# Performance work log

Hardware: AMD Instinct MI355X
Metric: run time of the kernel (lower is better)

## Reference

```python
import jax, jax.numpy as jnp
import numpy as np

DIM = 1024
HEADS = 16
HIDDEN = 4 * DIM


def layernorm(x, g, b, eps=1e-5):
    mu = jnp.mean(x, axis=-1, keepdims=True)
    var = jnp.mean(jnp.square(x - mu), axis=-1, keepdims=True)
    return (x - mu) * jax.lax.rsqrt(var + eps) * g + b


def setup_inputs() -> dict:
    key = jax.random.key(0)
    ks = jax.random.split(key, 8)
    s = DIM ** -0.5
    return {
        "x": jax.random.normal(ks[0], (2, 2048, DIM), dtype=jnp.float32),
        "ln1_g": jnp.ones((DIM,), jnp.float32),
        "ln1_b": jnp.zeros((DIM,), jnp.float32),
        "qkv_w": jax.random.normal(ks[1], (DIM, 3 * DIM), jnp.float32) * s,
        "proj_w": jax.random.normal(ks[2], (DIM, DIM), jnp.float32) * s,
        "proj_b": jnp.zeros((DIM,), jnp.float32),
        "ln2_g": jnp.ones((DIM,), jnp.float32),
        "ln2_b": jnp.zeros((DIM,), jnp.float32),
        "fc1_w": jax.random.normal(ks[3], (DIM, HIDDEN), jnp.float32) * s,
        "fc1_b": jnp.zeros((HIDDEN,), jnp.float32),
        "fc2_w": jax.random.normal(ks[4], (HIDDEN, DIM), jnp.float32) * (HIDDEN ** -0.5),
        "fc2_b": jnp.zeros((DIM,), jnp.float32),
    }


def block_fwd(x, ln1_g, ln1_b, qkv_w, proj_w, proj_b, ln2_g, ln2_b,
              fc1_w, fc1_b, fc2_w, fc2_b):
    B, N, C = x.shape
    H = HEADS
    Dh = C // H
    scale = Dh ** -0.5
    # --- attention branch (pre-norm) ---
    h = layernorm(x, ln1_g, ln1_b)
    qkv = h @ qkv_w                     # [B,N,3C] (no bias: qkv_bias=False)
    qkv = qkv.reshape(B, N, 3, H, Dh)
    q = qkv[:, :, 0].transpose(0, 2, 1, 3)   # [B,H,N,Dh]
    k = qkv[:, :, 1].transpose(0, 2, 1, 3)
    v = qkv[:, :, 2].transpose(0, 2, 1, 3)
    attn = jnp.einsum('bhqd,bhkd->bhqk', q, k) * scale
    attn = jax.nn.softmax(attn, axis=-1)
    o = jnp.einsum('bhqk,bhkd->bhqd', attn, v)
    o = o.transpose(0, 2, 1, 3).reshape(B, N, C)
    x = x + (o @ proj_w + proj_b)
    # --- MLP branch (pre-norm) ---
    h = layernorm(x, ln2_g, ln2_b)
    h = jax.nn.gelu(h @ fc1_w + fc1_b, approximate=False)  # torch nn.GELU = exact erf
    x = x + (h @ fc2_w + fc2_b)
    return x


def reference(x, ln1_g, ln1_b, qkv_w, proj_w, proj_b, ln2_g, ln2_b,
              fc1_w, fc1_b, fc2_w, fc2_b):
    return block_fwd(x, ln1_g, ln1_b, qkv_w, proj_w, proj_b, ln2_g, ln2_b,
                     fc1_w, fc1_b, fc2_w, fc2_b)
```

## Files before the change

kernel.cpp:

```cpp
#include <hip/hip_runtime.h>
#include <math.h>

typedef unsigned short u16;
typedef unsigned int u32;
typedef __attribute__((ext_vector_type(8))) short short8;
typedef __attribute__((ext_vector_type(4))) float f32x4;
typedef __attribute__((ext_vector_type(16))) float f32x16;
typedef __attribute__((ext_vector_type(2))) u32 u32x2;
typedef __attribute__((ext_vector_type(4))) u32 u32x4;
typedef __attribute__((ext_vector_type(4))) u16 u16x4;

typedef __attribute__((address_space(1))) const void gmem_t;
typedef __attribute__((address_space(3))) void lmem_t;

__device__ __forceinline__ u16 f2bf(float f) {
  u32 u = __builtin_bit_cast(u32, f);
  u = u + 0x7fffu + ((u >> 16) & 1u);
  return (u16)(u >> 16);
}

__device__ __forceinline__ u32 cvt_pk_bf16(float a, float b) {
  u32 r;
  asm("v_cvt_pk_bf16_f32 %0, %1, %2" : "=v"(r) : "v"(a), "v"(b));
  return r;
}

__device__ __forceinline__ void g2l16(const void* g, void* l) {
  __builtin_amdgcn_global_load_lds((gmem_t*)g, (lmem_t*)l, 16, 0, 0);
}

template <int N> __device__ __forceinline__ void waitcnt_vm() {
  if constexpr (N == 0)      asm volatile("s_waitcnt vmcnt(0)" ::: "memory");
  else if constexpr (N == 4) asm volatile("s_waitcnt vmcnt(4)" ::: "memory");
  else if constexpr (N == 6) asm volatile("s_waitcnt vmcnt(6)" ::: "memory");
  else if constexpr (N == 8) asm volatile("s_waitcnt vmcnt(8)" ::: "memory");
  else static_assert(N == 0 || N == 4 || N == 6 || N == 8, "add literal");
}

__global__ __launch_bounds__(256) void wtrans_all(
    const float* __restrict__ qkvw, const float* __restrict__ projw,
    const float* __restrict__ fc1w, const float* __restrict__ fc2w,
    u16* __restrict__ o_qkv, u16* __restrict__ o_proj,
    u16* __restrict__ o_fc1, u16* __restrict__ o_fc2) {
  int id = (int)blockIdx.x;
  const float* in; u16* out; int R, C, bid;
  if (id < 768)       { in = qkvw;  out = o_qkv;  R = 1024; C = 3072; bid = id; }
  else if (id < 1024) { in = projw; out = o_proj; R = 1024; C = 1024; bid = id - 768; }
  else if (id < 2048) { in = fc1w;  out = o_fc1;  R = 1024; C = 4096; bid = id - 1024; }
  else                { in = fc2w;  out = o_fc2;  R = 4096; C = 1024; bid = id - 2048; }
  __shared__ float t[64][65];
  int tid = threadIdx.x;
  int nbx = C >> 6;
  int bx = bid % nbx, by = bid / nbx;
  int r0 = by << 6, c0 = bx << 6;
  int lr = tid >> 2, lc = (tid & 3) << 4;
  const float* src = in + (size_t)(r0 + lr) * C + c0 + lc;
#pragma unroll
  for (int j = 0; j < 4; ++j) {
    f32x4 v = *(const f32x4*)(src + j * 4);
    t[lr][lc + j * 4 + 0] = v.x; t[lr][lc + j * 4 + 1] = v.y;
    t[lr][lc + j * 4 + 2] = v.z; t[lr][lc + j * 4 + 3] = v.w;
  }
  __syncthreads();
  int oc = tid >> 2, orr = (tid & 3) << 4;
  u16* dst = out + (size_t)(c0 + oc) * R + r0 + orr;
  u32 u[8];
#pragma unroll
  for (int j = 0; j < 8; ++j)
    u[j] = (u32)f2bf(t[orr + 2 * j][oc]) | ((u32)f2bf(t[orr + 2 * j + 1][oc]) << 16);
  u32x4 v0; v0.x = u[0]; v0.y = u[1]; v0.z = u[2]; v0.w = u[3];
  u32x4 v1; v1.x = u[4]; v1.y = u[5]; v1.z = u[6]; v1.w = u[7];
  *(u32x4*)(dst) = v0;
  *(u32x4*)(dst + 8) = v1;
}

__global__ __launch_bounds__(256) void lnorm(const float* __restrict__ in,
                                             const float* __restrict__ gw,
                                             const float* __restrict__ bw,
                                             u16* __restrict__ out) {
  int r = blockIdx.x, tid = threadIdx.x;
  const f32x4 v = *((const f32x4*)(in + (size_t)r * 1024) + tid);
  float s = v.x + v.y + v.z + v.w;
  float ss = v.x * v.x + v.y * v.y + v.z * v.z + v.w * v.w;
#pragma unroll
  for (int o = 32; o >= 1; o >>= 1) { s += __shfl_xor(s, o); ss += __shfl_xor(ss, o); }
  __shared__ float red[8];
  int w = tid >> 6;
  if ((tid & 63) == 0) { red[w] = s; red[4 + w] = ss; }
  __syncthreads();
  s = red[0] + red[1] + red[2] + red[3];
  ss = red[4] + red[5] + red[6] + red[7];
  float mu = s * (1.0f / 1024.0f);
  float var = ss * (1.0f / 1024.0f) - mu * mu;
  float rstd = rsqrtf(var + 1e-5f);
  const f32x4 g4 = *((const f32x4*)gw + tid);
  const f32x4 b4 = *((const f32x4*)bw + tid);
  u16x4 o;
  o.x = f2bf((v.x - mu) * rstd * g4.x + b4.x);
  o.y = f2bf((v.y - mu) * rstd * g4.y + b4.y);
  o.z = f2bf((v.z - mu) * rstd * g4.z + b4.z);
  o.w = f2bf((v.w - mu) * rstd * g4.w + b4.w);
  *((u16x4*)(out + (size_t)r * 1024) + tid) = o;
}

template <int EPI, int BM, int BN>
__global__ __launch_bounds__(256, 2) void gemm_bt(
    const u16* __restrict__ A, const u16* __restrict__ BT, int M, int N, int K,
    const float* __restrict__ bias, const float* __restrict__ resid,
    float* __restrict__ fout, u16* __restrict__ bout) {
  constexpr int AIT = BM / 32, BIT = BN / 32;
  constexpr int L = AIT + BIT;
  constexpr int MR = BM / 32, NR = BN / 32;
  __shared__ __align__(16) u16 smA[2][BM * 64];
  __shared__ __align__(16) u16 smB[2][BN * 64];
  int tid = threadIdx.x;
  int w = tid >> 6, l = tid & 63, lq = l & 15, g = l >> 4;
  int nbx = N / BN;
  int t = (int)blockIdx.x;
  int cpx = (int)gridDim.x >> 3;
  t = (t & 7) * cpx + (t >> 3);
  int by = t / nbx, bx = t - by * nbx;
  long brow = (long)by * BM, bcol = (long)bx * BN;
  int wr = w >> 1, wc = w & 1;

  const u16* aS[AIT]; const u16* bS[BIT];
#pragma unroll
  for (int it = 0; it < AIT; ++it) {
    int p = it * 256 + tid;
    int row = p >> 3;
    int gc = (p & 7) ^ (row & 7);
    aS[it] = A + (size_t)(brow + row) * K + gc * 8;
  }
#pragma unroll
  for (int it = 0; it < BIT; ++it) {
    int p = it * 256 + tid;
    int row = p >> 3;
    int gc = (p & 7) ^ (row & 7);
    bS[it] = BT + (size_t)(bcol + row) * K + gc * 8;
  }
  auto STAGE = [&](int buf, int k0) {
#pragma unroll
    for (int it = 0; it < AIT; ++it) g2l16(aS[it] + k0, &smA[buf][it * 2048 + w * 512]);
#pragma unroll
    for (int it = 0; it < BIT; ++it) g2l16(bS[it] + k0, &smB[buf][it * 2048 + w * 512]);
  };

  f32x4 zero = {0.f, 0.f, 0.f, 0.f};
  f32x4 acc[MR][NR];
#pragma unroll
  for (int m = 0; m < MR; ++m)
#pragma unroll
    for (int n = 0; n < NR; ++n) acc[m][n] = zero;

  int NT = K >> 6;
  STAGE(0, 0);
  for (int tt = 0; tt < NT; ++tt) {
    int cur = tt & 1;
    int knext = ((tt + 1) == NT ? 0 : (tt + 1)) << 6;
    STAGE(cur ^ 1, knext);
    waitcnt_vm<L>();
    __builtin_amdgcn_s_barrier();
    asm volatile("" ::: "memory");

    const char* sA = (const char*)&smA[cur][0];
    const char* sB = (const char*)&smB[cur][0];
#pragma unroll
    for (int c = 0; c < 2; ++c) {
      short8 af[MR], bfb[NR];
#pragma unroll
      for (int m = 0; m < MR; ++m) {
        int r = wr * (BM / 2) + m * 16 + lq;
        af[m] = *(const short8*)(sA + r * 128 + ((g * 16 + c * 64) ^ ((r & 7) << 4)));
      }
#pragma unroll
      for (int n = 0; n < NR; ++n) {
        int r = wc * (BN / 2) + n * 16 + lq;
        bfb[n] = *(const short8*)(sB + r * 128 + ((g * 16 + c * 64) ^ ((r & 7) << 4)));
      }
#pragma unroll
      for (int m = 0; m < MR; ++m)
#pragma unroll
        for (int n = 0; n < NR; ++n)
          acc[m][n] = __builtin_amdgcn_mfma_f32_16x16x32_bf16(af[m], bfb[n], acc[m][n], 0, 0, 0);
    }
    asm volatile("" ::: "memory");
    __builtin_amdgcn_s_barrier();
  }
  waitcnt_vm<0>();

  long colbase = bcol + wc * (BN / 2);
#pragma unroll
  for (int m = 0; m < MR; ++m) {
#pragma unroll
    for (int n = 0; n < NR; ++n) {
      f32x4 v = acc[m][n];
      long col = colbase + n * 16 + lq;
      long row0 = brow + wr * (BM / 2) + m * 16 + g * 4;
      float bb = bias[col];
#pragma unroll
      for (int i = 0; i < 4; ++i) {
        long idx = (row0 + i) * N + col;
        fout[idx] = resid[idx] + v[i] + bb;
      }
    }
  }
}

template <int EPI>
__global__ __launch_bounds__(256, 4) void gemm32(
    const u16* __restrict__ A, const u16* __restrict__ BT, int M, int N, int K,
    const float* __restrict__ bias,
    u16* __restrict__ bout, u16* __restrict__ bout2, u16* __restrict__ bout3) {
  __shared__ __align__(16) u16 smA[2][128 * 32];
  __shared__ __align__(16) u16 smB[2][128 * 32];
  int tid = threadIdx.x;
  int w = tid >> 6, l = tid & 63, lq = l & 15, g = l >> 4;
  int nbx = N >> 7;
  int t = (int)blockIdx.x;
  int cpx = (int)gridDim.x >> 3;
  t = (t & 7) * cpx + (t >> 3);
  int by = t / nbx, bx = t - by * nbx;
  long brow = (long)by << 7, bcol = (long)bx << 7;
  int wr = w >> 1, wc = w & 1;

  const u16* aS[2]; const u16* bS[2];
#pragma unroll
  for (int it = 0; it < 2; ++it) {
    int p = it * 256 + tid;
    int sp = (p & 7) ^ ((p >> 3) & 7);
    int row = ((p >> 3) << 1) | (sp >> 2);
    int c = sp & 3;
    aS[it] = A + (size_t)(brow + row) * K + c * 8;
    bS[it] = BT + (size_t)(bcol + row) * K + c * 8;
  }
  auto STAGE = [&](int buf, int k0) {
#pragma unroll
    for (int it = 0; it < 2; ++it) {
      g2l16(aS[it] + k0, &smA[buf][it * 2048 + w * 512]);
      g2l16(bS[it] + k0, &smB[buf][it * 2048 + w * 512]);
    }
  };

  f32x4 zero = {0.f, 0.f, 0.f, 0.f};
  f32x4 acc[4][4];
#pragma unroll
  for (int m = 0; m < 4; ++m)
#pragma unroll
    for (int n = 0; n < 4; ++n) acc[m][n] = zero;

  int NT = K >> 5;
  STAGE(0, 0);
  for (int tt = 0; tt < NT; ++tt) {
    int cur = tt & 1;
    int knext = ((tt + 1) == NT ? 0 : (tt + 1)) << 5;
    STAGE(cur ^ 1, knext);
    waitcnt_vm<4>();
    __builtin_amdgcn_s_barrier();
    asm volatile("" ::: "memory");

    const char* sA = (const char*)&smA[cur][0];
    const char* sB = (const char*)&smB[cur][0];
    short8 af[4], bfb[4];
#pragma unroll
    for (int m = 0; m < 4; ++m) {
      int r = wr * 64 + m * 16 + lq;
      af[m] = *(const short8*)(sA + ((r >> 1) * 128 +
                ((((r & 1) << 6) + (g << 4)) ^ (((r >> 1) & 7) << 4))));
    }
#pragma unroll
    for (int n = 0; n < 4; ++n) {
      int r = wc * 64 + n * 16 + lq;
      bfb[n] = *(const short8*)(sB + ((r >> 1) * 128 +
                ((((r & 1) << 6) + (g << 4)) ^ (((r >> 1) & 7) << 4))));
    }
    __builtin_amdgcn_s_setprio(1);
#pragma unroll
    for (int m = 0; m < 4; ++m)
#pragma unroll
      for (int n = 0; n < 4; ++n)
        acc[m][n] = __builtin_amdgcn_mfma_f32_16x16x32_bf16(af[m], bfb[n], acc[m][n], 0, 0, 0);
    __builtin_amdgcn_s_setprio(0);
    asm volatile("" ::: "memory");
    __builtin_amdgcn_s_barrier();
  }
  waitcnt_vm<0>();

#pragma unroll
  for (int m = 0; m < 4; ++m) {
#pragma unroll
    for (int n = 0; n < 4; ++n) {
      f32x4 v = acc[m][n];
      long col = bcol + wc * 64 + n * 16 + lq;
      long row0 = brow + wr * 64 + m * 16 + g * 4;
      if constexpr (EPI == 0) {
        int part = (int)(bcol >> 10);
        long colq = col - ((long)part << 10);
        int hh = (int)(colq >> 6), d = (int)(colq & 63);
#pragma unroll
        for (int i = 0; i < 4; ++i) {
          long row = row0 + i;
          long b = row >> 11, nq = row & 2047;
          long bh = b * 16 + hh;
          u16 val = f2bf(v[i]);
          if (part == 0)      bout [(bh * 2048 + nq) * 64 + d] = val;
          else if (part == 1) bout2[(bh * 2048 + nq) * 64 + d] = val;
          else                bout3[(bh * 64 + d) * 2048 + nq] = val;
        }
      } else {
        float bb = bias[col];
#pragma unroll
        for (int i = 0; i < 4; ++i) {
          float xg = v[i] + bb;
          float ge = 0.5f * xg * (1.0f + erff(xg * 0.70710678118654752f));
          bout[(row0 + i) * (long)N + col] = f2bf(ge);
        }
      }
    }
  }
}

template <int BASE>
__device__ __forceinline__ short8 mk_pfrag(const f32x16& s, float sc) {
  u32 x = cvt_pk_bf16(exp2f(s[BASE + 0] * sc - 12.0f), exp2f(s[BASE + 1] * sc - 12.0f));
  u32 y = cvt_pk_bf16(exp2f(s[BASE + 2] * sc - 12.0f), exp2f(s[BASE + 3] * sc - 12.0f));
  u32 u = cvt_pk_bf16(exp2f(s[BASE + 4] * sc - 12.0f), exp2f(s[BASE + 5] * sc - 12.0f));
  u32 v = cvt_pk_bf16(exp2f(s[BASE + 6] * sc - 12.0f), exp2f(s[BASE + 7] * sc - 12.0f));
  asm("v_permlane32_swap_b32 %0, %1" : "+v"(x), "+v"(u));
  asm("v_permlane32_swap_b32 %0, %1" : "+v"(y), "+v"(v));
  u32x4 f; f.x = x; f.y = y; f.z = u; f.w = v;
  return __builtin_bit_cast(short8, f);
}

__global__ __launch_bounds__(256, 2) void attn_fwd(const u16* __restrict__ qb,
                                                   const u16* __restrict__ kbuf,
                                                   const u16* __restrict__ vtb,
                                                   u16* __restrict__ ob) {
  __shared__ __align__(16) u16 kl[2][64 * 64];
  __shared__ __align__(16) u16 vl[2][64 * 64];
  int tid = threadIdx.x;
  int w = tid >> 6, l = tid & 63, q32 = l & 31, hi = l >> 5;
  int bh = (int)blockIdx.x & 31;
  int qt = (int)blockIdx.x >> 5;

  const u16* qp = qb + ((size_t)bh * 2048 + qt * 128 + w * 32 + q32) * 64 + hi * 8;
  short8 qf[4];
#pragma unroll
  for (int kc = 0; kc < 4; ++kc) qf[kc] = *(const short8*)(qp + kc * 16);

  const u16* kS[2]; const u16* vS[2];
#pragma unroll
  for (int it = 0; it < 2; ++it) {
    int p = it * 256 + tid;
    int row = p >> 3;
    int gc = (p & 7) ^ (row & 7);
    kS[it] = kbuf + ((size_t)bh * 2048 + row) * 64 + gc * 8;
    vS[it] = vtb + ((size_t)bh * 64 + row) * 2048 + gc * 8;
  }
  auto issue = [&](int buf, int kt0) {
#pragma unroll
    for (int it = 0; it < 2; ++it) {
      g2l16(kS[it] + (size_t)kt0 * 64, &kl[buf][it * 2048 + w * 512]);
      g2l16(vS[it] + kt0,              &vl[buf][it * 2048 + w * 512]);
    }
  };

  f32x16 z16 = {0,0,0,0,0,0,0,0,0,0,0,0,0,0,0,0};
  f32x16 accO0 = z16, accO1 = z16, accl = z16;
  const float sc = 0.125f * 1.44269504088896f;
  u32x4 ov; ov.x = ov.y = ov.z = ov.w = 0x3F803F80u;
  short8 onesf = __builtin_bit_cast(short8, ov);
  int swz = (q32 & 7) << 4;

  issue(0, 0);
  for (int t = 0; t < 32; ++t) {
    int cur = t & 1;
    issue(cur ^ 1, ((t + 1) & 31) << 6);
    waitcnt_vm<4>();
    __builtin_amdgcn_s_barrier();
    asm volatile("" ::: "memory");

    const char* klc = (const char*)&kl[cur][0];
    const char* vlc = (const char*)&vl[cur][0];

    f32x16 s0 = z16, s1 = z16;
    __builtin_amdgcn_s_setprio(1);
#pragma unroll
    for (int kc = 0; kc < 4; ++kc) {
      short8 k0 = *(const short8*)(klc + (q32 * 128 +        ((kc * 32 + hi * 16) ^ swz)));
      short8 k1 = *(const short8*)(klc + ((32 + q32) * 128 + ((kc * 32 + hi * 16) ^ swz)));
      s0 = __builtin_amdgcn_mfma_f32_32x32x16_bf16(k0, qf[kc], s0, 0, 0, 0);
      s1 = __builtin_amdgcn_mfma_f32_32x32x16_bf16(k1, qf[kc], s1, 0, 0, 0);
    }
    __builtin_amdgcn_s_setprio(0);

    short8 pf0 = mk_pfrag<0>(s0, sc);
    short8 pf1 = mk_pfrag<8>(s0, sc);
    short8 pf2 = mk_pfrag<0>(s1, sc);
    short8 pf3 = mk_pfrag<8>(s1, sc);

    short8 va0[4], va1[4];
#pragma unroll
    for (int c = 0; c < 4; ++c) {
      va0[c] = *(const short8*)(vlc + (q32 * 128 +        ((c * 32 + hi * 16) ^ swz)));
      va1[c] = *(const short8*)(vlc + ((32 + q32) * 128 + ((c * 32 + hi * 16) ^ swz)));
    }
    __builtin_amdgcn_s_setprio(1);
    accO0 = __builtin_amdgcn_mfma_f32_32x32x16_bf16(va0[0], pf0, accO0, 0, 0, 0);
    accO1 = __builtin_amdgcn_mfma_f32_32x32x16_bf16(va1[0], pf0, accO1, 0, 0, 0);
    accl  = __builtin_amdgcn_mfma_f32_32x32x16_bf16(onesf,  pf0, accl,  0, 0, 0);
    accO0 = __builtin_amdgcn_mfma_f32_32x32x16_bf16(va0[1], pf1, accO0, 0, 0, 0);
    accO1 = __builtin_amdgcn_mfma_f32_32x32x16_bf16(va1[1], pf1, accO1, 0, 0, 0);
    accl  = __builtin_amdgcn_mfma_f32_32x32x16_bf16(onesf,  pf1, accl,  0, 0, 0);
    accO0 = __builtin_amdgcn_mfma_f32_32x32x16_bf16(va0[2], pf2, accO0, 0, 0, 0);
    accO1 = __builtin_amdgcn_mfma_f32_32x32x16_bf16(va1[2], pf2, accO1, 0, 0, 0);
    accl  = __builtin_amdgcn_mfma_f32_32x32x16_bf16(onesf,  pf2, accl,  0, 0, 0);
    accO0 = __builtin_amdgcn_mfma_f32_32x32x16_bf16(va0[3], pf3, accO0, 0, 0, 0);
    accO1 = __builtin_amdgcn_mfma_f32_32x32x16_bf16(va1[3], pf3, accO1, 0, 0, 0);
    accl  = __builtin_amdgcn_mfma_f32_32x32x16_bf16(onesf,  pf3, accl,  0, 0, 0);
    __builtin_amdgcn_s_setprio(0);

    asm volatile("" ::: "memory");
    __builtin_amdgcn_s_barrier();
  }
  waitcnt_vm<0>();

  float li = 1.0f / accl[0];
  int b = bh >> 4, h = bh & 15;
  long q = (long)qt * 128 + w * 32 + q32;
  u16* obase = ob + ((long)b * 2048 + q) * 1024 + h * 64;
#pragma unroll
  for (int j = 0; j < 8; ++j) {
    int d = ((2 * j) & 3) + 8 * (j >> 1) + 4 * hi;
    *(u32*)(obase + d)      = cvt_pk_bf16(accO0[2 * j] * li, accO0[2 * j + 1] * li);
    *(u32*)(obase + 32 + d) = cvt_pk_bf16(accO1[2 * j] * li, accO1[2 * j + 1] * li);
  }
}

extern "C" void kernel_launch(void* const* d_in, const int* in_sizes, int n_in,
                              void* d_out, int out_size, void* d_ws, size_t ws_size,
                              hipStream_t stream) {
  const float* x     = (const float*)d_in[0];
  const float* ln1g  = (const float*)d_in[1];
  const float* ln1b  = (const float*)d_in[2];
  const float* qkvw  = (const float*)d_in[3];
  const float* projw = (const float*)d_in[4];
  const float* projb = (const float*)d_in[5];
  const float* ln2g  = (const float*)d_in[6];
  const float* ln2b  = (const float*)d_in[7];
  const float* fc1w  = (const float*)d_in[8];
  const float* fc1b  = (const float*)d_in[9];
  const float* fc2w  = (const float*)d_in[10];
  const float* fc2b  = (const float*)d_in[11];
  char* ws = (char*)d_ws;
  u16* qkv_wt  = (u16*)(ws + 0);
  u16* proj_wt = (u16*)(ws + 6291456);
  u16* fc1_wt  = (u16*)(ws + 8388608);
  u16* fc2_wt  = (u16*)(ws + 16777216);
  u16* h       = (u16*)(ws + 25165824);
  u16* qbuf    = (u16*)(ws + 33554432);
  u16* kbuf    = (u16*)(ws + 41943040);
  u16* vtbuf   = (u16*)(ws + 50331648);
  u16* aout    = (u16*)(ws + 58720256);
  float* y1    = (float*)(ws + 67108864);
  u16* gbuf    = (u16*)(ws + 33554432);
  float* outp  = (float*)d_out;

  wtrans_all<<<3072, 256, 0, stream>>>(qkvw, projw, fc1w, fc2w,
                                       qkv_wt, proj_wt, fc1_wt, fc2_wt);

  lnorm<<<4096, 256, 0, stream>>>(x, ln1g, ln1b, h);
  gemm32<0><<<768, 256, 0, stream>>>(h, qkv_wt, 4096, 3072, 1024,
                                     nullptr, qbuf, kbuf, vtbuf);
  attn_fwd<<<512, 256, 0, stream>>>(qbuf, kbuf, vtbuf, aout);
  gemm_bt<1, 64, 128><<<512, 256, 0, stream>>>(aout, proj_wt, 4096, 1024, 1024,
                                               projb, x, y1, nullptr);
  lnorm<<<4096, 256, 0, stream>>>(y1, ln2g, ln2b, h);
  gemm32<2><<<1024, 256, 0, stream>>>(h, fc1_wt, 4096, 4096, 1024,
                                      fc1b, gbuf, nullptr, nullptr);
  gemm_bt<3, 64, 128><<<512, 256, 0, stream>>>(gbuf, fc2_wt, 4096, 1024, 4096,
                                               fc2b, y1, outp, nullptr);
}
```

Baseline: 246.1 us.

## Split attention over key halves and add a combine kernel

Attention blocks now each process half of the key sequence, doubling the grid so more blocks are resident per CU, and write unnormalised bf16 partial outputs plus row sums to scratch. A new combine kernel sums the two partials and normalises. The softmax scale is folded into Q during the QKV GEMM epilogue, removing a multiply-add per score. This adds an extra launch, a scratch write and read of the partial outputs, and a small extra bf16 rounding of the partials.

```diff
diff --git a/kernel.cpp b/kernel.cpp
--- a/kernel.cpp
+++ b/kernel.cpp
@@ -36,6 +36,8 @@
   else if constexpr (N == 8) asm volatile("s_waitcnt vmcnt(8)" ::: "memory");
   else static_assert(N == 0 || N == 4 || N == 6 || N == 8, "add literal");
 }
+
+#define QSCALE 0.1803368801111204f
 
 __global__ __launch_bounds__(256) void wtrans_all(
     const float* __restrict__ qkvw, const float* __restrict__ projw,
@@ -301,10 +303,9 @@
           long row = row0 + i;
           long b = row >> 11, nq = row & 2047;
           long bh = b * 16 + hh;
-          u16 val = f2bf(v[i]);
-          if (part == 0)      bout [(bh * 2048 + nq) * 64 + d] = val;
-          else if (part == 1) bout2[(bh * 2048 + nq) * 64 + d] = val;
-          else                bout3[(bh * 64 + d) * 2048 + nq] = val;
+          if (part == 0)      bout [(bh * 2048 + nq) * 64 + d] = f2bf(v[i] * QSCALE);
+          else if (part == 1) bout2[(bh * 2048 + nq) * 64 + d] = f2bf(v[i]);
+          else                bout3[(bh * 64 + d) * 2048 + nq] = f2bf(v[i]);
         }
       } else {
         float bb = bias[col];
@@ -320,27 +321,30 @@
 }
 
 template <int BASE>
-__device__ __forceinline__ short8 mk_pfrag(const f32x16& s, float sc) {
-  u32 x = cvt_pk_bf16(exp2f(s[BASE + 0] * sc - 12.0f), exp2f(s[BASE + 1] * sc - 12.0f));
-  u32 y = cvt_pk_bf16(exp2f(s[BASE + 2] * sc - 12.0f), exp2f(s[BASE + 3] * sc - 12.0f));
-  u32 u = cvt_pk_bf16(exp2f(s[BASE + 4] * sc - 12.0f), exp2f(s[BASE + 5] * sc - 12.0f));
-  u32 v = cvt_pk_bf16(exp2f(s[BASE + 6] * sc - 12.0f), exp2f(s[BASE + 7] * sc - 12.0f));
+__device__ __forceinline__ short8 mk_pfrag(const f32x16& s) {
+  u32 x = cvt_pk_bf16(exp2f(s[BASE + 0]), exp2f(s[BASE + 1]));
+  u32 y = cvt_pk_bf16(exp2f(s[BASE + 2]), exp2f(s[BASE + 3]));
+  u32 u = cvt_pk_bf16(exp2f(s[BASE + 4]), exp2f(s[BASE + 5]));
+  u32 v = cvt_pk_bf16(exp2f(s[BASE + 6]), exp2f(s[BASE + 7]));
   asm("v_permlane32_swap_b32 %0, %1" : "+v"(x), "+v"(u));
   asm("v_permlane32_swap_b32 %0, %1" : "+v"(y), "+v"(v));
   u32x4 f; f.x = x; f.y = y; f.z = u; f.w = v;
   return __builtin_bit_cast(short8, f);
 }
 
-__global__ __launch_bounds__(256, 2) void attn_fwd(const u16* __restrict__ qb,
+__global__ __launch_bounds__(256, 4) void attn_fwd(const u16* __restrict__ qb,
                                                    const u16* __restrict__ kbuf,
                                                    const u16* __restrict__ vtb,
-                                                   u16* __restrict__ ob) {
+                                                   u16* __restrict__ po,
+                                                   float* __restrict__ plb) {
   __shared__ __align__(16) u16 kl[2][64 * 64];
   __shared__ __align__(16) u16 vl[2][64 * 64];
   int tid = threadIdx.x;
   int w = tid >> 6, l = tid & 63, q32 = l & 31, hi = l >> 5;
-  int bh = (int)blockIdx.x & 31;
-  int qt = (int)blockIdx.x >> 5;
+  int bidx = (int)blockIdx.x;
+  int bh = bidx & 31;
+  int qt = (bidx >> 5) & 15;
+  int half = bidx >> 9;
 
   const u16* qp = qb + ((size_t)bh * 2048 + qt * 128 + w * 32 + q32) * 64 + hi * 8;
   short8 qf[4];
@@ -366,15 +370,15 @@
 
   f32x16 z16 = {0,0,0,0,0,0,0,0,0,0,0,0,0,0,0,0};
   f32x16 accO0 = z16, accO1 = z16, accl = z16;
-  const float sc = 0.125f * 1.44269504088896f;
   u32x4 ov; ov.x = ov.y = ov.z = ov.w = 0x3F803F80u;
   short8 onesf = __builtin_bit_cast(short8, ov);
   int swz = (q32 & 7) << 4;
-
-  issue(0, 0);
-  for (int t = 0; t < 32; ++t) {
+  int tbase = half << 4;
+
+  issue(0, tbase << 6);
+  for (int t = 0; t < 16; ++t) {
     int cur = t & 1;
-    issue(cur ^ 1, ((t + 1) & 31) << 6);
+    issue(cur ^ 1, (tbase + ((t + 1) & 15)) << 6);
     waitcnt_vm<4>();
     __builtin_amdgcn_s_barrier();
     asm volatile("" ::: "memory");
@@ -393,10 +397,10 @@
     }
     __builtin_amdgcn_s_setprio(0);
 
-    short8 pf0 = mk_pfrag<0>(s0, sc);
-    short8 pf1 = mk_pfrag<8>(s0, sc);
-    short8 pf2 = mk_pfrag<0>(s1, sc);
-    short8 pf3 = mk_pfrag<8>(s1, sc);
+    short8 pf0 = mk_pfrag<0>(s0);
+    short8 pf1 = mk_pfrag<8>(s0);
+    short8 pf2 = mk_pfrag<0>(s1);
+    short8 pf3 = mk_pfrag<8>(s1);
 
     short8 va0[4], va1[4];
 #pragma unroll
@@ -424,16 +428,47 @@
   }
   waitcnt_vm<0>();
 
-  float li = 1.0f / accl[0];
   int b = bh >> 4, h = bh & 15;
   long q = (long)qt * 128 + w * 32 + q32;
-  u16* obase = ob + ((long)b * 2048 + q) * 1024 + h * 64;
+  u16* pbase = po + (size_t)half * 4194304 + ((long)b * 2048 + q) * 1024 + h * 64;
 #pragma unroll
   for (int j = 0; j < 8; ++j) {
     int d = ((2 * j) & 3) + 8 * (j >> 1) + 4 * hi;
-    *(u32*)(obase + d)      = cvt_pk_bf16(accO0[2 * j] * li, accO0[2 * j + 1] * li);
-    *(u32*)(obase + 32 + d) = cvt_pk_bf16(accO1[2 * j] * li, accO1[2 * j + 1] * li);
-  }
+    *(u32*)(pbase + d)      = cvt_pk_bf16(accO0[2 * j], accO0[2 * j + 1]);
+    *(u32*)(pbase + 32 + d) = cvt_pk_bf16(accO1[2 * j], accO1[2 * j + 1]);
+  }
+  if (hi == 0)
+    plb[(half << 16) + (bh << 11) + (int)q] = accl[0];
+}
+
+__global__ __launch_bounds__(256) void attn_combine(const u16* __restrict__ po,
+                                                    const float* __restrict__ plb,
+                                                    u16* __restrict__ aout) {
+  int i = (int)blockIdx.x * 256 + threadIdx.x;
+  int row = i >> 7;
+  int c8 = (i & 127) << 3;
+  int b = row >> 11, q = row & 2047, h = c8 >> 6;
+  int bh = b * 16 + h;
+  float l0 = plb[(bh << 11) + q];
+  float l1 = plb[(1 << 16) + (bh << 11) + q];
+  float li = 1.0f / (l0 + l1);
+  const u16x4* p0 = (const u16x4*)(po + (size_t)row * 1024 + c8);
+  const u16x4* p1 = (const u16x4*)(po + 4194304 + (size_t)row * 1024 + c8);
+  u32 out[4];
+#pragma unroll
+  for (int k = 0; k < 2; ++k) {
+    u16x4 a = p0[k], bv = p1[k];
+#pragma unroll
+    for (int j = 0; j < 4; j += 2) {
+      float x0 = __builtin_bit_cast(float, (u32)a[j] << 16) +
+                 __builtin_bit_cast(float, (u32)bv[j] << 16);
+      float x1 = __builtin_bit_cast(float, (u32)a[j + 1] << 16) +
+                 __builtin_bit_cast(float, (u32)bv[j + 1] << 16);
+      out[k * 2 + j / 2] = cvt_pk_bf16(x0 * li, x1 * li);
+    }
+  }
+  u32x4 ov; ov.x = out[0]; ov.y = out[1]; ov.z = out[2]; ov.w = out[3];
+  *(u32x4*)(aout + (size_t)row * 1024 + c8) = ov;
 }
 
 extern "C" void kernel_launch(void* const* d_in, const int* in_sizes, int n_in,
@@ -464,6 +499,8 @@
   float* y1    = (float*)(ws + 67108864);
   u16* gbuf    = (u16*)(ws + 33554432);
   float* outp  = (float*)d_out;
+  u16* po      = (u16*)y1;
+  float* plb   = (float*)h;
 
   wtrans_all<<<3072, 256, 0, stream>>>(qkvw, projw, fc1w, fc2w,
                                        qkv_wt, proj_wt, fc1_wt, fc2_wt);
@@ -471,7 +508,8 @@
   lnorm<<<4096, 256, 0, stream>>>(x, ln1g, ln1b, h);
   gemm32<0><<<768, 256, 0, stream>>>(h, qkv_wt, 4096, 3072, 1024,
                                      nullptr, qbuf, kbuf, vtbuf);
-  attn_fwd<<<512, 256, 0, stream>>>(qbuf, kbuf, vtbuf, aout);
+  attn_fwd<<<1024, 256, 0, stream>>>(qbuf, kbuf, vtbuf, po, plb);
+  attn_combine<<<2048, 256, 0, stream>>>(po, plb, aout);
   gemm_bt<1, 64, 128><<<512, 256, 0, stream>>>(aout, proj_wt, 4096, 1024, 1024,
                                                projb, x, y1, nullptr);
   lnorm<<<4096, 256, 0, stream>>>(y1, ln2g, ln2b, h);
```

After: 256.5 us. 4.2% more time.
